# Kernel optimization log

Hardware: AMD Instinct MI355X
Metric: run time of the kernel (lower is better)

## Reference

```python
import jax, jax.numpy as jnp
import numpy as np

CIN, HID, OUT = 64, 64, 128
BB, NN, KK = 8, 2048, 16
EPS = 1e-5


def _bn(t, g, b):
    # BatchNorm1d in training mode on (B, n, C): per-channel stats over (B, n), biased var
    mu = t.mean(axis=(0, 1))
    var = t.var(axis=(0, 1))
    return (t - mu) * jax.lax.rsqrt(var + EPS) * g + b


def setup_inputs() -> dict:
    key = jax.random.key(0)
    ks = jax.random.split(key, 12)
    N = BB * NN
    E = N * KK
    x = jax.random.normal(ks[0], (N, CIN), dtype=jnp.float32)
    p = jax.random.normal(ks[1], (N, 3), dtype=jnp.float32)
    sid_euc = jax.random.randint(ks[2], (E,), 0, N)
    tid_euc = jnp.repeat(jnp.arange(N), KK)  # tid_euc[::k] == arange(N)
    s_in = 1.0 / np.sqrt(CIN)
    s_hid = 1.0 / np.sqrt(HID)
    return {
        'x': x, 'p': p, 'sid_euc': sid_euc, 'tid_euc': tid_euc,
        'B': BB, 'n': NN,
        'lins_W': jax.random.normal(ks[3], (6, CIN, HID), dtype=jnp.float32) * s_in,
        'lins_b': jax.random.normal(ks[4], (6, HID), dtype=jnp.float32) * s_in,
        'lin1_W': jax.random.normal(ks[5], (CIN, OUT), dtype=jnp.float32) * s_in,
        'lin1_b': jax.random.normal(ks[6], (OUT,), dtype=jnp.float32) * s_in,
        'lin2_W': jax.random.normal(ks[7], (HID, OUT), dtype=jnp.float32) * s_hid,
        'lin2_b': jax.random.normal(ks[8], (OUT,), dtype=jnp.float32) * s_hid,
        'g1': jnp.ones((HID,), jnp.float32), 'b1': jnp.zeros((HID,), jnp.float32),
        'g2': jnp.ones((OUT,), jnp.float32), 'b2': jnp.zeros((OUT,), jnp.float32),
    }


def reference(x, p, sid_euc, tid_euc, B, n, lins_W, lins_b, lin1_W, lin1_b,
              lin2_W, lin2_b, g1, b1, g2, b2):
    E = sid_euc.shape[0]
    k = E // (B * n)
    edge = x[sid_euc] - x[tid_euc]                       # [E, Cin]
    p_diff = p[sid_euc] - p[tid_euc]                     # [E, 3]
    p_dis = jnp.maximum(jnp.linalg.norm(p_diff, axis=-1, keepdims=True), 1e-16)
    p_cos = jnp.cos(p_diff / p_dis) ** 2                 # [E, 3]
    p_cos = p_cos.T.reshape(3, B, n, k, 1)
    bid = (p_diff > 0).astype(jnp.int32) + jnp.array([0, 2, 4], dtype=jnp.int32)  # [E,3]
    # all 6 experts densely, then per-edge per-axis selection (faithful to original)
    edge6 = jnp.einsum('ec,sch->seh', edge, lins_W) + lins_b[:, None, :]          # [6,E,H]
    sel = edge6[bid.T, jnp.arange(E)[None, :]]            # [3, E, H]
    sel = sel.reshape(3, B, n, k, -1) * p_cos
    e = sel.sum(axis=0)                                   # [B, n, k, H]
    pd = p_dis.reshape(B, n, k, 1)
    p_r = pd.max(axis=2, keepdims=True) * 1.1
    p_d = (p_r - pd) ** 2
    e = e * p_d / p_d.sum(axis=2, keepdims=True)
    y = e.sum(axis=2)                                     # [B, n, H]
    y = jax.nn.relu(_bn(y, g1, b1))
    xr = x[tid_euc[::k]] @ lin1_W + lin1_b                # [B*n, Out]
    y = xr.reshape(B, n, -1) + (y @ lin2_W + lin2_b)
    y = jax.nn.relu(_bn(y, g2, b2))
    return y.reshape(B * n, -1)
```

## Files before the change

kernel.cpp:

```cpp
#include <hip/hip_runtime.h>
#include <hip/hip_bf16.h>

#define NNODES 16384
#define KEDGE  16
#define EPS    1e-5f


#define SP1_OFF 0
#define SP2_OFF (SP1_OFF + 8*128)
#define WF_OFF  (SP2_OFF + 8*256)
#define Y1_OFF  (WF_OFF + 12288)
#define T2_OFF  (Y1_OFF + NNODES*64)

typedef __attribute__((ext_vector_type(8))) short bf16x8;
typedef __attribute__((ext_vector_type(4))) float f32x4;

__device__ __forceinline__ short f2bf(float f) {
    const unsigned u = __float_as_uint(f);
    return (short)((u + 0x7fffu + ((u >> 16) & 1u)) >> 16);
}

__global__ __launch_bounds__(256) void k_prep(
    const float* __restrict__ W, short* __restrict__ Wfrag,
    float* __restrict__ sp)
{
    const int idx = blockIdx.x * 256 + threadIdx.x;
    if (idx < 24576) {
        const int j  = idx & 7;
        const int l  = (idx >> 3) & 63;
        const int r  = idx >> 9;
        const int kt = r % 12;
        const int w  = r / 12;
        const int k  = kt*32 + (l >> 4)*8 + j;
        const int n  = w*16 + (l & 15);
        Wfrag[idx] = f2bf(W[k*64 + n]);
    } else if (idx - 24576 < 3072) {
        sp[idx - 24576] = 0.f;
    }
}

__global__ __launch_bounds__(256, 4) void k_node(
    const float* __restrict__ x, const float* __restrict__ p,
    const int* __restrict__ sid,
    const short* __restrict__ Wfrag, const float* __restrict__ bias,
    float* __restrict__ y1, float* __restrict__ sp1)
{
    __shared__ float  Ash[16][396];
    __shared__ float4 Esh[4][64];

    const int lane = threadIdx.x & 63;
    const int wv   = threadIdx.x >> 6;
    const int tw   = blockIdx.x * 16 + wv * 4;

    const int ii = lane >> 4;
    const int t1 = tw + ii;
    const int s  = sid[t1 * KEDGE + (lane & 15)];
    const float ptx = p[t1*3+0], pty = p[t1*3+1], ptz = p[t1*3+2];
    const float dx = p[s*3+0] - ptx;
    const float dy = p[s*3+1] - pty;
    const float dz = p[s*3+2] - ptz;
    float pd = fmaxf(sqrtf(dx*dx + dy*dy + dz*dz), 1e-16f);

    float pr = pd;
    pr = fmaxf(pr, __shfl_xor(pr, 1));
    pr = fmaxf(pr, __shfl_xor(pr, 2));
    pr = fmaxf(pr, __shfl_xor(pr, 4));
    pr = fmaxf(pr, __shfl_xor(pr, 8));
    pr *= 1.1f;

    float w = (pr - pd) * (pr - pd);
    float wsum = w;
    wsum += __shfl_xor(wsum, 1);
    wsum += __shfl_xor(wsum, 2);
    wsum += __shfl_xor(wsum, 4);
    wsum += __shfl_xor(wsum, 8);
    w /= wsum;

    const float invd = 1.f / pd;
    const float c0 = __cosf(dx * invd);
    const float c1 = __cosf(dy * invd);
    const float c2 = __cosf(dz * invd);
    const int flags = (dx > 0.f ? 1 : 0) | (dy > 0.f ? 2 : 0) | (dz > 0.f ? 4 : 0);
    Esh[wv][lane] = make_float4(w * c0 * c0, w * c1 * c1, w * c2 * c2,
                                __int_as_float((s << 3) | flags));

    #pragma unroll
    for (int i = 0; i < 4; ++i) {
        const float xt = x[(tw + i)*64 + lane];

        float ev[KEDGE];
        #pragma unroll
        for (int j = 0; j < KEDGE; ++j) {
            const int sv = __shfl(s, i*16 + j);
            ev[j] = x[sv*64 + lane];
        }

        float A0=0,A1=0,A2=0,A3=0,A4=0,A5=0;
        float B0=0,B1=0,B2=0,B3=0,B4=0,B5=0;
        #pragma unroll
        for (int j = 0; j < KEDGE; ++j) {
            const float4 pk = Esh[wv][i*16 + j];
            const int f = __builtin_amdgcn_readfirstlane(__float_as_int(pk.w)) & 7;
            const float e = ev[j] - xt;
            if (f & 1) { A1 += pk.x*e; B1 += pk.x; } else { A0 += pk.x*e; B0 += pk.x; }
            if (f & 2) { A3 += pk.y*e; B3 += pk.y; } else { A2 += pk.y*e; B2 += pk.y; }
            if (f & 4) { A5 += pk.z*e; B5 += pk.z; } else { A4 += pk.z*e; B4 += pk.z; }
        }
        const int r = wv*4 + i;
        Ash[r][0*64+lane] = A0; Ash[r][1*64+lane] = A1; Ash[r][2*64+lane] = A2;
        Ash[r][3*64+lane] = A3; Ash[r][4*64+lane] = A4; Ash[r][5*64+lane] = A5;
        if (lane == 0) {
            Ash[r][384] = B0; Ash[r][385] = B1; Ash[r][386] = B2;
            Ash[r][387] = B3; Ash[r][388] = B4; Ash[r][389] = B5;
        }
    }
    __syncthreads();

    const int m    = lane & 15;
    const int quad = lane >> 4;
    f32x4 acc = {0.f, 0.f, 0.f, 0.f};
    const short* wf = Wfrag + ((size_t)(wv*12)*64 + lane)*8;
    #pragma unroll
    for (int kt = 0; kt < 12; ++kt) {
        const float4 fa = *(const float4*)&Ash[m][kt*32 + quad*8];
        const float4 fb = *(const float4*)&Ash[m][kt*32 + quad*8 + 4];
        bf16x8 a;
        a[0]=f2bf(fa.x); a[1]=f2bf(fa.y); a[2]=f2bf(fa.z); a[3]=f2bf(fa.w);
        a[4]=f2bf(fb.x); a[5]=f2bf(fb.y); a[6]=f2bf(fb.z); a[7]=f2bf(fb.w);
        const bf16x8 b = *(const bf16x8*)(wf + (size_t)kt*64*8);
        acc = __builtin_amdgcn_mfma_f32_16x16x32_bf16(a, b, acc, 0, 0, 0);
    }

    const int n = wv*16 + m;
    float bvv[6];
    #pragma unroll
    for (int s6 = 0; s6 < 6; ++s6) bvv[s6] = bias[s6*64 + n];

    float sloc = 0.f, qloc = 0.f;
    #pragma unroll
    for (int r = 0; r < 4; ++r) {
        const int mr = quad*4 + r;
        const float4 be  = *(const float4*)&Ash[mr][384];
        const float2 be2 = *(const float2*)&Ash[mr][388];
        float yv = acc[r]
                 + be.x*bvv[0] + be.y*bvv[1] + be.z*bvv[2] + be.w*bvv[3]
                 + be2.x*bvv[4] + be2.y*bvv[5];
        y1[(size_t)(blockIdx.x*16 + mr)*64 + n] = yv;
        sloc += yv; qloc += yv*yv;
    }
    sloc += __shfl_xor(sloc, 16); sloc += __shfl_xor(sloc, 32);
    qloc += __shfl_xor(qloc, 16); qloc += __shfl_xor(qloc, 32);
    if (lane < 16) {
        atomicAdd(&sp1[(blockIdx.x & 7)*128 + n],      sloc);
        atomicAdd(&sp1[(blockIdx.x & 7)*128 + 64 + n], qloc);
    }
}

#define MAC4(Wm, kk, c)                                   \
    {                                                     \
        const float wa = Wm[(kk)*128 + lane];             \
        const float wb = Wm[(kk)*128 + 64 + lane];        \
        a0[0] += r0v.c*wa; a1[0] += r0v.c*wb;             \
        a0[1] += r1v.c*wa; a1[1] += r1v.c*wb;             \
        a0[2] += r2v.c*wa; a1[2] += r2v.c*wb;             \
        a0[3] += r3v.c*wa; a1[3] += r3v.c*wb;             \
    }

__global__ __launch_bounds__(256, 3) void k_fused2(
    const float* __restrict__ x,
    const float* __restrict__ y1, const float* __restrict__ sp1,
    const float* __restrict__ g1, const float* __restrict__ b1,
    const float* __restrict__ W1, const float* __restrict__ bias1,
    const float* __restrict__ W2, const float* __restrict__ bias2,
    float* __restrict__ t2, float* __restrict__ sp2)
{
    __shared__ float st1sh[128];
    __shared__ float Zsh[16][68];
    __shared__ float Xsh[16][68];
    __shared__ float redsh[1024];

    const int lane = threadIdx.x & 63;
    const int wv   = threadIdx.x >> 6;
    const int r0   = (blockIdx.x * 4 + wv) * 4;

    if (threadIdx.x < 128) {
        float v = 0.f;
        #pragma unroll
        for (int s8 = 0; s8 < 8; ++s8) v += sp1[s8*128 + threadIdx.x];
        st1sh[threadIdx.x] = v;
    }
    __syncthreads();

    const float n_inv = 1.f / NNODES;
    const float mu  = st1sh[lane] * n_inv;
    const float var = st1sh[64 + lane] * n_inv - mu*mu;
    const float sc  = rsqrtf(var + EPS) * g1[lane];
    const float sh  = b1[lane] - mu*sc;

    const int rb = wv * 4;
    #pragma unroll
    for (int i = 0; i < 4; ++i) {
        Xsh[rb+i][lane] = x[(size_t)(r0 + i)*64 + lane];
        const float yv = y1[(r0 + i)*64 + lane];
        Zsh[rb+i][lane] = fmaxf(yv*sc + sh, 0.f);
    }

    float a0[4] = {0,0,0,0}, a1[4] = {0,0,0,0};
    #pragma unroll 2
    for (int k = 0; k < 64; k += 4) {
        const float4 r0v = *(const float4*)&Zsh[rb+0][k];
        const float4 r1v = *(const float4*)&Zsh[rb+1][k];
        const float4 r2v = *(const float4*)&Zsh[rb+2][k];
        const float4 r3v = *(const float4*)&Zsh[rb+3][k];
        MAC4(W2, k+0, x)
        MAC4(W2, k+1, y)
        MAC4(W2, k+2, z)
        MAC4(W2, k+3, w)
    }
    #pragma unroll 2
    for (int k = 0; k < 64; k += 4) {
        const float4 r0v = *(const float4*)&Xsh[rb+0][k];
        const float4 r1v = *(const float4*)&Xsh[rb+1][k];
        const float4 r2v = *(const float4*)&Xsh[rb+2][k];
        const float4 r3v = *(const float4*)&Xsh[rb+3][k];
        MAC4(W1, k+0, x)
        MAC4(W1, k+1, y)
        MAC4(W1, k+2, z)
        MAC4(W1, k+3, w)
    }
    const float bb0 = bias1[lane]      + bias2[lane];
    const float bb1 = bias1[64 + lane] + bias2[64 + lane];
    float s0=0,q0=0,s1=0,q1=0;
    #pragma unroll
    for (int i = 0; i < 4; ++i) {
        const float v0 = a0[i] + bb0;
        const float v1 = a1[i] + bb1;
        t2[(size_t)(r0 + i)*128 + lane]      = v0;
        t2[(size_t)(r0 + i)*128 + 64 + lane] = v1;
        s0 += v0; q0 += v0*v0;
        s1 += v1; q1 += v1*v1;
    }
    redsh[wv*256 + lane]       = s0;
    redsh[wv*256 + 64 + lane]  = s1;
    redsh[wv*256 + 128 + lane] = q0;
    redsh[wv*256 + 192 + lane] = q1;
    __syncthreads();
    {
        const int t = threadIdx.x;
        const float v = redsh[t] + redsh[256+t] + redsh[512+t] + redsh[768+t];
        atomicAdd(&sp2[(blockIdx.x & 7)*256 + t], v);
    }
}

__global__ __launch_bounds__(256) void k_bn2(
    const float* __restrict__ t2, const float* __restrict__ sp2,
    const float* __restrict__ g2, const float* __restrict__ b2,
    float* __restrict__ out)
{
    __shared__ float st2sh[256];
    {
        float v = 0.f;
        #pragma unroll
        for (int s8 = 0; s8 < 8; ++s8) v += sp2[s8*256 + threadIdx.x];
        st2sh[threadIdx.x] = v;
    }
    __syncthreads();

    const int i4 = blockIdx.x * 256 + threadIdx.x;
    const int c4 = i4 & 31;
    const float4 sum4 = ((const float4*)st2sh)[c4];
    const float4 sq4  = ((const float4*)(st2sh + 128))[c4];
    const float4 g4   = ((const float4*)g2)[c4];
    const float4 bb4  = ((const float4*)b2)[c4];
    const float4 v    = ((const float4*)t2)[i4];
    const float n_inv = 1.f / NNODES;
    float4 o;
    {
        const float m = sum4.x*n_inv, va = sq4.x*n_inv - m*m;
        const float scv = rsqrtf(va + EPS)*g4.x;
        o.x = fmaxf(v.x*scv + (bb4.x - m*scv), 0.f);
    }
    {
        const float m = sum4.y*n_inv, va = sq4.y*n_inv - m*m;
        const float scv = rsqrtf(va + EPS)*g4.y;
        o.y = fmaxf(v.y*scv + (bb4.y - m*scv), 0.f);
    }
    {
        const float m = sum4.z*n_inv, va = sq4.z*n_inv - m*m;
        const float scv = rsqrtf(va + EPS)*g4.z;
        o.z = fmaxf(v.z*scv + (bb4.z - m*scv), 0.f);
    }
    {
        const float m = sum4.w*n_inv, va = sq4.w*n_inv - m*m;
        const float scv = rsqrtf(va + EPS)*g4.w;
        o.w = fmaxf(v.w*scv + (bb4.w - m*scv), 0.f);
    }
    ((float4*)out)[i4] = o;
}

extern "C" void kernel_launch(void* const* d_in, const int* in_sizes, int n_in,
                              void* d_out, int out_size, void* d_ws, size_t ws_size,
                              hipStream_t stream)
{
    const float* x     = (const float*)d_in[0];
    const float* p     = (const float*)d_in[1];
    const int*   sid   = (const int*)d_in[2];
    const float* linsW = (const float*)d_in[6];
    const float* linsB = (const float*)d_in[7];
    const float* W1    = (const float*)d_in[8];
    const float* b1l   = (const float*)d_in[9];
    const float* W2    = (const float*)d_in[10];
    const float* b2l   = (const float*)d_in[11];
    const float* g1    = (const float*)d_in[12];
    const float* bb1   = (const float*)d_in[13];
    const float* g2    = (const float*)d_in[14];
    const float* bb2   = (const float*)d_in[15];

    float* ws    = (float*)d_ws;
    float* sp1   = ws + SP1_OFF;
    float* sp2   = ws + SP2_OFF;
    short* wfrag = (short*)(ws + WF_OFF);
    float* y1    = ws + Y1_OFF;
    float* t2    = ws + T2_OFF;

    k_prep  <<<108,                  256, 0, stream>>>(linsW, wfrag, sp1);
    k_node  <<<NNODES/16,            256, 0, stream>>>(x, p, sid, wfrag,
                                                       linsB, y1, sp1);
    k_fused2<<<NNODES/16,            256, 0, stream>>>(x, y1, sp1, g1, bb1,
                                                       W1, b1l, W2, b2l, t2, sp2);
    k_bn2   <<<(NNODES*128)/(256*4), 256, 0, stream>>>(t2, sp2, g2, bb2,
                                                       (float*)d_out);
}
```

Baseline: 132.4 us.

## Use bf16 MFMA for the fused lin1/lin2 GEMM in k_fused2

Replaces the scalar FP32 FMA loops for x@W1 and z@W2 in the second fused kernel with bf16 16x16x32 MFMA instructions. W1 and W2 are pre-converted into MFMA fragment layout in the prep kernel, and the workspace is enlarged to hold them. The per-block shared-memory reduction for BN2 stats becomes cross-lane shuffles plus atomics, and occupancy is raised to 4 blocks. This lowers precision of the output GEMM to bf16 inputs, which is a numerical risk.

After: 121.8 us. 8.0% less time.

```diff
diff --git a/kernel.cpp b/kernel.cpp
--- a/kernel.cpp
+++ b/kernel.cpp
@@ -9,7 +9,7 @@
 #define SP1_OFF 0
 #define SP2_OFF (SP1_OFF + 8*128)
 #define WF_OFF  (SP2_OFF + 8*256)
-#define Y1_OFF  (WF_OFF + 12288)
+#define Y1_OFF  (WF_OFF + 28672)
 #define T2_OFF  (Y1_OFF + NNODES*64)
 
 typedef __attribute__((ext_vector_type(8))) short bf16x8;
@@ -21,7 +21,8 @@
 }
 
 __global__ __launch_bounds__(256) void k_prep(
-    const float* __restrict__ W, short* __restrict__ Wfrag,
+    const float* __restrict__ W, const float* __restrict__ W1,
+    const float* __restrict__ W2, short* __restrict__ Wfrag,
     float* __restrict__ sp)
 {
     const int idx = blockIdx.x * 256 + threadIdx.x;
@@ -34,8 +35,19 @@
         const int k  = kt*32 + (l >> 4)*8 + j;
         const int n  = w*16 + (l & 15);
         Wfrag[idx] = f2bf(W[k*64 + n]);
-    } else if (idx - 24576 < 3072) {
-        sp[idx - 24576] = 0.f;
+    } else if (idx < 24576 + 32768) {
+        const int i2 = idx - 24576;
+        const int j  = i2 & 7;
+        const int l  = (i2 >> 3) & 63;
+        const int r  = i2 >> 9;
+        const int kt = r & 1;
+        const int nt = (r >> 1) & 7;
+        const float* Ws = (r >> 4) ? W2 : W1;
+        const int k  = kt*32 + (l >> 4)*8 + j;
+        const int n  = nt*16 + (l & 15);
+        Wfrag[idx] = f2bf(Ws[k*128 + n]);
+    } else if (idx - 57344 < 3072) {
+        sp[idx - 57344] = 0.f;
     }
 }
 
@@ -156,28 +168,17 @@
     }
 }
 
-#define MAC4(Wm, kk, c)                                   \
-    {                                                     \
-        const float wa = Wm[(kk)*128 + lane];             \
-        const float wb = Wm[(kk)*128 + 64 + lane];        \
-        a0[0] += r0v.c*wa; a1[0] += r0v.c*wb;             \
-        a0[1] += r1v.c*wa; a1[1] += r1v.c*wb;             \
-        a0[2] += r2v.c*wa; a1[2] += r2v.c*wb;             \
-        a0[3] += r3v.c*wa; a1[3] += r3v.c*wb;             \
-    }
-
-__global__ __launch_bounds__(256, 3) void k_fused2(
+__global__ __launch_bounds__(256, 4) void k_fused2(
     const float* __restrict__ x,
     const float* __restrict__ y1, const float* __restrict__ sp1,
     const float* __restrict__ g1, const float* __restrict__ b1,
-    const float* __restrict__ W1, const float* __restrict__ bias1,
-    const float* __restrict__ W2, const float* __restrict__ bias2,
+    const short* __restrict__ WfragF,
+    const float* __restrict__ bias1, const float* __restrict__ bias2,
     float* __restrict__ t2, float* __restrict__ sp2)
 {
     __shared__ float st1sh[128];
     __shared__ float Zsh[16][68];
     __shared__ float Xsh[16][68];
-    __shared__ float redsh[1024];
 
     const int lane = threadIdx.x & 63;
     const int wv   = threadIdx.x >> 6;
@@ -204,51 +205,58 @@
         const float yv = y1[(r0 + i)*64 + lane];
         Zsh[rb+i][lane] = fmaxf(yv*sc + sh, 0.f);
     }
-
-    float a0[4] = {0,0,0,0}, a1[4] = {0,0,0,0};
-    #pragma unroll 2
-    for (int k = 0; k < 64; k += 4) {
-        const float4 r0v = *(const float4*)&Zsh[rb+0][k];
-        const float4 r1v = *(const float4*)&Zsh[rb+1][k];
-        const float4 r2v = *(const float4*)&Zsh[rb+2][k];
-        const float4 r3v = *(const float4*)&Zsh[rb+3][k];
-        MAC4(W2, k+0, x)
-        MAC4(W2, k+1, y)
-        MAC4(W2, k+2, z)
-        MAC4(W2, k+3, w)
-    }
-    #pragma unroll 2
-    for (int k = 0; k < 64; k += 4) {
-        const float4 r0v = *(const float4*)&Xsh[rb+0][k];
-        const float4 r1v = *(const float4*)&Xsh[rb+1][k];
-        const float4 r2v = *(const float4*)&Xsh[rb+2][k];
-        const float4 r3v = *(const float4*)&Xsh[rb+3][k];
-        MAC4(W1, k+0, x)
-        MAC4(W1, k+1, y)
-        MAC4(W1, k+2, z)
-        MAC4(W1, k+3, w)
-    }
-    const float bb0 = bias1[lane]      + bias2[lane];
-    const float bb1 = bias1[64 + lane] + bias2[64 + lane];
-    float s0=0,q0=0,s1=0,q1=0;
-    #pragma unroll
-    for (int i = 0; i < 4; ++i) {
-        const float v0 = a0[i] + bb0;
-        const float v1 = a1[i] + bb1;
-        t2[(size_t)(r0 + i)*128 + lane]      = v0;
-        t2[(size_t)(r0 + i)*128 + 64 + lane] = v1;
-        s0 += v0; q0 += v0*v0;
-        s1 += v1; q1 += v1*v1;
-    }
-    redsh[wv*256 + lane]       = s0;
-    redsh[wv*256 + 64 + lane]  = s1;
-    redsh[wv*256 + 128 + lane] = q0;
-    redsh[wv*256 + 192 + lane] = q1;
     __syncthreads();
-    {
-        const int t = threadIdx.x;
-        const float v = redsh[t] + redsh[256+t] + redsh[512+t] + redsh[768+t];
-        atomicAdd(&sp2[(blockIdx.x & 7)*256 + t], v);
+
+    const int m    = lane & 15;
+    const int quad = lane >> 4;
+    f32x4 accA = {0.f,0.f,0.f,0.f}, accB = {0.f,0.f,0.f,0.f};
+    const int ntA = wv*2, ntB = wv*2 + 1;
+    #pragma unroll
+    for (int kt = 0; kt < 2; ++kt) {
+        const float4 xa = *(const float4*)&Xsh[m][kt*32 + quad*8];
+        const float4 xb = *(const float4*)&Xsh[m][kt*32 + quad*8 + 4];
+        bf16x8 ax;
+        ax[0]=f2bf(xa.x); ax[1]=f2bf(xa.y); ax[2]=f2bf(xa.z); ax[3]=f2bf(xa.w);
+        ax[4]=f2bf(xb.x); ax[5]=f2bf(xb.y); ax[6]=f2bf(xb.z); ax[7]=f2bf(xb.w);
+        const bf16x8 b1A = *(const bf16x8*)(WfragF + ((size_t)(((0*8+ntA)*2+kt)*64 + lane))*8);
+        const bf16x8 b1B = *(const bf16x8*)(WfragF + ((size_t)(((0*8+ntB)*2+kt)*64 + lane))*8);
+        accA = __builtin_amdgcn_mfma_f32_16x16x32_bf16(ax, b1A, accA, 0, 0, 0);
+        accB = __builtin_amdgcn_mfma_f32_16x16x32_bf16(ax, b1B, accB, 0, 0, 0);
+        const float4 za = *(const float4*)&Zsh[m][kt*32 + quad*8];
+        const float4 zb = *(const float4*)&Zsh[m][kt*32 + quad*8 + 4];
+        bf16x8 az;
+        az[0]=f2bf(za.x); az[1]=f2bf(za.y); az[2]=f2bf(za.z); az[3]=f2bf(za.w);
+        az[4]=f2bf(zb.x); az[5]=f2bf(zb.y); az[6]=f2bf(zb.z); az[7]=f2bf(zb.w);
+        const bf16x8 b2A = *(const bf16x8*)(WfragF + ((size_t)(((1*8+ntA)*2+kt)*64 + lane))*8);
+        const bf16x8 b2B = *(const bf16x8*)(WfragF + ((size_t)(((1*8+ntB)*2+kt)*64 + lane))*8);
+        accA = __builtin_amdgcn_mfma_f32_16x16x32_bf16(az, b2A, accA, 0, 0, 0);
+        accB = __builtin_amdgcn_mfma_f32_16x16x32_bf16(az, b2B, accB, 0, 0, 0);
+    }
+
+    const int nA = wv*32 + m, nB = wv*32 + 16 + m;
+    const float bbA = bias1[nA] + bias2[nA];
+    const float bbB = bias1[nB] + bias2[nB];
+    float sA=0,qA=0,sB=0,qB=0;
+    #pragma unroll
+    for (int r = 0; r < 4; ++r) {
+        const int mr = quad*4 + r;
+        const float vA = accA[r] + bbA;
+        const float vB = accB[r] + bbB;
+        t2[(size_t)(blockIdx.x*16 + mr)*128 + nA] = vA;
+        t2[(size_t)(blockIdx.x*16 + mr)*128 + nB] = vB;
+        sA += vA; qA += vA*vA;
+        sB += vB; qB += vB*vB;
+    }
+    sA += __shfl_xor(sA, 16); sA += __shfl_xor(sA, 32);
+    qA += __shfl_xor(qA, 16); qA += __shfl_xor(qA, 32);
+    sB += __shfl_xor(sB, 16); sB += __shfl_xor(sB, 32);
+    qB += __shfl_xor(qB, 16); qB += __shfl_xor(qB, 32);
+    if (lane < 16) {
+        float* slot = sp2 + (blockIdx.x & 7)*256;
+        atomicAdd(&slot[nA],       sA);
+        atomicAdd(&slot[nB],       sB);
+        atomicAdd(&slot[128 + nA], qA);
+        atomicAdd(&slot[128 + nB], qB);
     }
 }
 
@@ -323,11 +331,12 @@
     float* y1    = ws + Y1_OFF;
     float* t2    = ws + T2_OFF;
 
-    k_prep  <<<108,                  256, 0, stream>>>(linsW, wfrag, sp1);
+    k_prep  <<<236,                  256, 0, stream>>>(linsW, W1, W2, wfrag, sp1);
     k_node  <<<NNODES/16,            256, 0, stream>>>(x, p, sid, wfrag,
                                                        linsB, y1, sp1);
     k_fused2<<<NNODES/16,            256, 0, stream>>>(x, y1, sp1, g1, bb1,
-                                                       W1, b1l, W2, b2l, t2, sp2);
+                                                       wfrag + 24576, b1l, b2l,
+                                                       t2, sp2);
     k_bn2   <<<(NNODES*128)/(256*4), 256, 0, stream>>>(t2, sp2, g2, bb2,
                                                        (float*)d_out);
 }
```
